# Kernel optimization log

Hardware: AMD Instinct MI355X
Metric: run time of the kernel (lower is better)

## Reference

```python
import jax, jax.numpy as jnp
import numpy as np

ALPHA = 0.2  # leaky relu slope
NEG_BIG = -9e15


def setup_inputs() -> dict:
    key = jax.random.key(0)
    k1, k2, k3, k4 = jax.random.split(key, 4)
    B, N, Fin, Fout = 8, 2048, 128, 128
    h = jax.random.normal(k1, (B, N, Fin), dtype=jnp.float32)
    adj = jax.random.randint(k2, (N, N), 0, 2, dtype=jnp.int32)
    # xavier_uniform with gain=1.414
    limW = 1.414 * np.sqrt(6.0 / (Fin + Fout))
    W = jax.random.uniform(k3, (Fin, Fout), minval=-limW, maxval=limW, dtype=jnp.float32)
    lima = 1.414 * np.sqrt(6.0 / (2 * Fout + 1))
    a = jax.random.uniform(k4, (2 * Fout, 1), minval=-lima, maxval=lima, dtype=jnp.float32)
    return {"h": h, "adj": adj, "W": W, "a": a}


def reference(h, adj, W, a):
    # Wh: [B, N, F]
    Wh = jnp.einsum("bnf,fo->bno", h, W)
    Fout = W.shape[1]
    a1, a2 = a[:Fout, 0], a[Fout:, 0]  # [F], [F]
    # Additive score decomposition (same math as concat trick):
    # e[b,i,j] = leakyrelu(Wh_i . a1 + Wh_j . a2)
    s1 = Wh @ a1  # [B, N] (source/query part)
    s2 = Wh @ a2  # [B, N] (target part)
    e = s1[:, :, None] + s2[:, None, :]  # [B, N, N]
    e = jnp.where(e > 0, e, ALPHA * e)   # leaky relu
    e = jnp.where(adj[None, :, :] > 0, e, NEG_BIG)
    attention = jax.nn.softmax(e, axis=2)  # [B, N, N]
    # dropout is identity in eval mode
    h_prime = jnp.einsum("bij,bjf->bif", attention, Wh)
    return h_prime
```

## Files before the change

### kernel.cpp

```cpp
#include <hip/hip_runtime.h>
#include <hip/hip_bf16.h>
#include <stdint.h>

#define ALPHA 0.2f

typedef __attribute__((ext_vector_type(8))) short bf16x8;
typedef __attribute__((ext_vector_type(4))) float f32x4;

__device__ __forceinline__ short f2bf(float f) {
    union { float f; uint32_t u; } c; c.f = f;
    uint32_t u = c.u + 0x7FFF + ((c.u >> 16) & 1);
    return (short)(u >> 16);
}

__device__ __forceinline__ uint32_t pk_bf16(float lo, float hi) {
    union { float f; uint32_t u; } a, b;
    a.f = lo; b.f = hi;
    return __builtin_amdgcn_perm(b.u + 0x8000u, a.u + 0x8000u, 0x07060302u);
}

__device__ __forceinline__ void gload_lds16(const void* g, void* l) {
    __builtin_amdgcn_global_load_lds(
        (const __attribute__((address_space(1))) void*)g,
        (__attribute__((address_space(3))) void*)l, 16, 0, 0);
}

__global__ __launch_bounds__(256) void pack_adj_kernel(
        const int* __restrict__ adj, uint8_t* __restrict__ bytes,
        const float* __restrict__ W, short* __restrict__ WTg) {
    int t = blockIdx.x * 256 + threadIdx.x;
    const int4* a4 = reinterpret_cast<const int4*>(adj) + (size_t)t * 2;
    int4 x0 = a4[0], x1 = a4[1];
    uint32_t m = 0;
    m |= (x0.x > 0) ? 1u   : 0u;  m |= (x0.y > 0) ? 2u   : 0u;
    m |= (x0.z > 0) ? 4u   : 0u;  m |= (x0.w > 0) ? 8u   : 0u;
    m |= (x1.x > 0) ? 16u  : 0u;  m |= (x1.y > 0) ? 32u  : 0u;
    m |= (x1.z > 0) ? 64u  : 0u;  m |= (x1.w > 0) ? 128u : 0u;
    bytes[t] = (uint8_t)m;

    if (blockIdx.x < 64) {
        int idx = blockIdx.x * 256 + threadIdx.x;
        int k = idx >> 7, f = idx & 127;
        WTg[f * 128 + k] = f2bf(W[k * 128 + f]);
    }
}

__global__ __launch_bounds__(256) void wh_kernel(
        const float* __restrict__ h, const short* __restrict__ WTg,
        const float* __restrict__ a, short* __restrict__ whT,
        float* __restrict__ s1g, float* __restrict__ s2g) {
    __shared__ float sred[4][2][16];
    __shared__ short tr[4][32][24];

    int tid = threadIdx.x, wid = tid >> 6, lane = tid & 63;
    int q = lane >> 4, n = lane & 15;
    int bb = blockIdx.x & 7;
    int tile = blockIdx.x >> 3;
    int rb = bb * 2048 + tile * 16;
    int row = rb + n;

    f32x4 acc[2] = {};
    #pragma unroll
    for (int kc = 0; kc < 4; ++kc) {
        const float* hp = h + (size_t)row * 128 + kc * 32 + q * 8;
        float4 h0 = reinterpret_cast<const float4*>(hp)[0];
        float4 h1 = reinterpret_cast<const float4*>(hp)[1];
        bf16x8 afrag;
        afrag[0] = f2bf(h0.x); afrag[1] = f2bf(h0.y);
        afrag[2] = f2bf(h0.z); afrag[3] = f2bf(h0.w);
        afrag[4] = f2bf(h1.x); afrag[5] = f2bf(h1.y);
        afrag[6] = f2bf(h1.z); afrag[7] = f2bf(h1.w);
        #pragma unroll
        for (int u = 0; u < 2; ++u) {
            int t = wid * 2 + u;
            bf16x8 bfrag = *reinterpret_cast<const bf16x8*>(
                WTg + (t * 16 + n) * 128 + kc * 32 + q * 8);
            acc[u] = __builtin_amdgcn_mfma_f32_16x16x32_bf16(afrag, bfrag, acc[u], 0, 0, 0);
        }
    }

    float p1[4] = {0.f, 0.f, 0.f, 0.f}, p2[4] = {0.f, 0.f, 0.f, 0.f};
    #pragma unroll
    for (int u = 0; u < 2; ++u) {
        int c = (wid * 2 + u) * 16 + n;
        float a1c = a[c], a2c = a[128 + c];
        #pragma unroll
        for (int r = 0; r < 4; ++r) {
            p1[r] += acc[u][r] * a1c;
            p2[r] += acc[u][r] * a2c;
        }
    }
    #pragma unroll
    for (int d = 1; d < 16; d <<= 1) {
        #pragma unroll
        for (int r = 0; r < 4; ++r) {
            p1[r] += __shfl_xor(p1[r], d);
            p2[r] += __shfl_xor(p2[r], d);
        }
    }
    if (n == 0) {
        #pragma unroll
        for (int r = 0; r < 4; ++r) {
            sred[wid][0][q * 4 + r] = p1[r];
            sred[wid][1][q * 4 + r] = p2[r];
        }
    }

    #pragma unroll
    for (int u = 0; u < 2; ++u)
        #pragma unroll
        for (int r = 0; r < 4; ++r)
            tr[wid][u * 16 + n][q * 4 + r] = f2bf(acc[u][r]);
    __syncthreads();

    if (wid == 0 && lane < 16) {
        float v1 = 0.f, v2 = 0.f;
        #pragma unroll
        for (int v = 0; v < 4; ++v) { v1 += sred[v][0][lane]; v2 += sred[v][1][lane]; }
        s1g[rb + lane] = v1;
        s2g[rb + lane] = v2;
    }

    int jr = rb & 2047;
    int fl = lane & 31, jh = lane >> 5;
    bf16x8 v = *reinterpret_cast<const bf16x8*>(&tr[wid][fl][jh * 8]);
    int f = wid * 32 + fl;
    int t = f >> 4, nn = f & 15;
    int jc = jr >> 5;
    int qg = ((jr & 31) >> 3) + jh;
    *reinterpret_cast<bf16x8*>(
        whT + (size_t)(bb * 64 + jc) * 4096 + t * 512 + qg * 128 + nn * 8) = v;
}

__global__ __launch_bounds__(256) void attn_kernel(
        const short* __restrict__ whT, const float* __restrict__ s1g,
        const float* __restrict__ s2g, const uint8_t* __restrict__ adjb,
        float* __restrict__ out) {
    __shared__ char sbuf[2][32768];

    int wid = threadIdx.x >> 6, lane = threadIdx.x & 63;
    int q = lane >> 4, n = lane & 15;
    int b  = blockIdx.x & 7;
    int ib = (blockIdx.x >> 3) * 64;
    int rowA = ib + wid * 16 + n;

    float s1A = s1g[b * 2048 + rowA];
    const float* s2b = s2g + b * 2048;
    const uint32_t* admA = reinterpret_cast<const uint32_t*>(
        adjb + (size_t)rowA * 256);
    const char* gbase = reinterpret_cast<const char*>(whT) + (size_t)b * 524288;

    f32x4 acc[8] = {};
    float ds = 0.f;

    uint32_t mw[4];
    float4 s2l[4], s2h[4];
    #pragma unroll
    for (int u = 0; u < 4; ++u) {
        mw[u] = admA[u];
        s2l[u] = *reinterpret_cast<const float4*>(s2b + u * 32 + q * 8);
        s2h[u] = *reinterpret_cast<const float4*>(s2b + u * 32 + q * 8 + 4);
    }

    {
        const char* g = gbase + wid * 8192 + lane * 16;
        char* l = &sbuf[0][wid * 8192];
        #pragma unroll
        for (int i = 0; i < 8; ++i)
            gload_lds16(g + i * 1024, l + i * 1024);
    }
    __syncthreads();

    for (int s = 0; s < 16; ++s) {
        int cur = s & 1;
        if (s < 15) {
            const char* g = gbase + (size_t)(s + 1) * 32768 + wid * 8192 + lane * 16;
            char* l = &sbuf[cur ^ 1][wid * 8192];
            #pragma unroll
            for (int i = 0; i < 8; ++i)
                gload_lds16(g + i * 1024, l + i * 1024);
        }
        const char* lb = sbuf[cur];
        #pragma unroll
        for (int u = 0; u < 4; ++u) {
            int c = s * 4 + u;
            bf16x8 nb[8];
            const char* cb = lb + u * 8192 + lane * 16;
            #pragma unroll
            for (int t = 0; t < 8; ++t)
                nb[t] = *reinterpret_cast<const bf16x8*>(cb + t * 1024);

            uint32_t mA = mw[u] >> (q * 8);
            float s2arr[8] = {s2l[u].x, s2l[u].y, s2l[u].z, s2l[u].w,
                              s2h[u].x, s2h[u].y, s2h[u].z, s2h[u].w};

            int cn = c + 4; if (cn > 63) cn = 63;
            mw[u] = admA[cn];
            s2l[u] = *reinterpret_cast<const float4*>(s2b + cn * 32 + q * 8);
            s2h[u] = *reinterpret_cast<const float4*>(s2b + cn * 32 + q * 8 + 4);

            float p[8];
            #pragma unroll
            for (int j = 0; j < 8; ++j) {
                float e = s1A + s2arr[j];
                e = fmaxf(e, ALPHA * e);
                float v = ((mA >> j) & 1) ? __expf(e) : 0.0f;
                ds += v; p[j] = v;
            }
            union { uint32_t u32[4]; bf16x8 v; } cv;
            #pragma unroll
            for (int pp = 0; pp < 4; ++pp)
                cv.u32[pp] = pk_bf16(p[2 * pp], p[2 * pp + 1]);

            #pragma unroll
            for (int t = 0; t < 8; ++t)
                acc[t] = __builtin_amdgcn_mfma_f32_16x16x32_bf16(cv.v, nb[t], acc[t], 0, 0, 0);
        }
        __syncthreads();
    }

    ds += __shfl_xor(ds, 16); ds += __shfl_xor(ds, 32);
    float rd[4];
    #pragma unroll
    for (int r = 0; r < 4; ++r) rd[r] = 1.0f / __shfl(ds, q * 4 + r);

    size_t ob = ((size_t)b * 2048 + ib + wid * 16) * 128;
    #pragma unroll
    for (int t = 0; t < 8; ++t)
        #pragma unroll
        for (int r = 0; r < 4; ++r)
            out[ob + (size_t)(q * 4 + r) * 128 + t * 16 + n] = acc[t][r] * rd[r];
}

extern "C" void kernel_launch(void* const* d_in, const int* in_sizes, int n_in,
                              void* d_out, int out_size, void* d_ws, size_t ws_size,
                              hipStream_t stream) {
    const float* h   = (const float*)d_in[0];
    const int*   adj = (const int*)d_in[1];
    const float* W   = (const float*)d_in[2];
    const float* a   = (const float*)d_in[3];
    float* out = (float*)d_out;

    char* ws = (char*)d_ws;
    short* whT = (short*)ws;
    float* s1  = (float*)(ws + 4194304);
    float* s2  = (float*)(ws + 4259840);
    uint8_t* bytes = (uint8_t*)(ws + 4325376);

    short* WTg = (short*)d_out + (4194304 - 16384);

    pack_adj_kernel<<<2048, 256, 0, stream>>>(adj, bytes, W, WTg);
    wh_kernel<<<1024, 256, 0, stream>>>(h, WTg, a, whT, s1, s2);
    attn_kernel<<<256, 256, 0, stream>>>(whT, s1, s2, bytes, out);
}
```

Measured before the change: 114.6 us.

## Stage adjacency mask and s2 in LDS and deepen whT pipeline to four stages

The attention kernel now preloads the block's 64 rows of packed adjacency bits and the full s2 vector into shared memory once, instead of issuing per-iteration global loads for them. The whT streaming changes from a double buffer of 32KB chunks to a 4-deep ring of 8KB chunks, with one chunk processed per iteration and manual vmcnt waits plus raw s_barrier in place of __syncthreads. The intent is to hide global-memory latency with finer-grained prefetch and fewer scalar/vector global loads in the inner loop. In exchange there are four times as many barriers, and correctness depends on the hand-written waitcnt counts, for example at the clamped tail where the last chunk is reloaded.

```diff
diff --git a/kernel.cpp b/kernel.cpp
--- a/kernel.cpp
+++ b/kernel.cpp
@@ -136,9 +136,11 @@
         const short* __restrict__ whT, const float* __restrict__ s1g,
         const float* __restrict__ s2g, const uint8_t* __restrict__ adjb,
         float* __restrict__ out) {
-    __shared__ char sbuf[2][32768];
-
-    int wid = threadIdx.x >> 6, lane = threadIdx.x & 63;
+    __shared__ char sbuf[4][8192];
+    __shared__ uint32_t mlds[64 * 65];
+    __shared__ float s2lds[2048];
+
+    int tid = threadIdx.x, wid = tid >> 6, lane = tid & 63;
     int q = lane >> 4, n = lane & 15;
     int b  = blockIdx.x & 7;
     int ib = (blockIdx.x >> 3) * 64;
@@ -146,77 +148,81 @@
 
     float s1A = s1g[b * 2048 + rowA];
     const float* s2b = s2g + b * 2048;
-    const uint32_t* admA = reinterpret_cast<const uint32_t*>(
-        adjb + (size_t)rowA * 256);
     const char* gbase = reinterpret_cast<const char*>(whT) + (size_t)b * 524288;
+
+    {
+        int rt = tid >> 2, seg = tid & 3;
+        const uint4* src = reinterpret_cast<const uint4*>(
+            adjb + (size_t)(ib + rt) * 256 + seg * 64);
+        uint32_t* dst = &mlds[rt * 65 + seg * 16];
+        #pragma unroll
+        for (int i = 0; i < 4; ++i) {
+            uint4 v = src[i];
+            dst[i * 4 + 0] = v.x; dst[i * 4 + 1] = v.y;
+            dst[i * 4 + 2] = v.z; dst[i * 4 + 3] = v.w;
+        }
+    }
+    {
+        float4 v0 = *reinterpret_cast<const float4*>(s2b + tid * 8);
+        float4 v1 = *reinterpret_cast<const float4*>(s2b + tid * 8 + 4);
+        *reinterpret_cast<float4*>(&s2lds[tid * 8])     = v0;
+        *reinterpret_cast<float4*>(&s2lds[tid * 8 + 4]) = v1;
+    }
+
+    #pragma unroll
+    for (int s0 = 0; s0 < 3; ++s0) {
+        const char* g = gbase + s0 * 8192 + wid * 2048 + lane * 16;
+        char* l = &sbuf[s0][wid * 2048];
+        gload_lds16(g, l);
+        gload_lds16(g + 1024, l + 1024);
+    }
+    asm volatile("s_waitcnt vmcnt(4) lgkmcnt(0)" ::: "memory");
+    asm volatile("s_barrier" ::: "memory");
 
     f32x4 acc[8] = {};
     float ds = 0.f;
-
-    uint32_t mw[4];
-    float4 s2l[4], s2h[4];
-    #pragma unroll
-    for (int u = 0; u < 4; ++u) {
-        mw[u] = admA[u];
-        s2l[u] = *reinterpret_cast<const float4*>(s2b + u * 32 + q * 8);
-        s2h[u] = *reinterpret_cast<const float4*>(s2b + u * 32 + q * 8 + 4);
-    }
-
-    {
-        const char* g = gbase + wid * 8192 + lane * 16;
-        char* l = &sbuf[0][wid * 8192];
-        #pragma unroll
-        for (int i = 0; i < 8; ++i)
-            gload_lds16(g + i * 1024, l + i * 1024);
-    }
-    __syncthreads();
-
-    for (int s = 0; s < 16; ++s) {
-        int cur = s & 1;
-        if (s < 15) {
-            const char* g = gbase + (size_t)(s + 1) * 32768 + wid * 8192 + lane * 16;
-            char* l = &sbuf[cur ^ 1][wid * 8192];
-            #pragma unroll
-            for (int i = 0; i < 8; ++i)
-                gload_lds16(g + i * 1024, l + i * 1024);
-        }
-        const char* lb = sbuf[cur];
-        #pragma unroll
-        for (int u = 0; u < 4; ++u) {
-            int c = s * 4 + u;
-            bf16x8 nb[8];
-            const char* cb = lb + u * 8192 + lane * 16;
-            #pragma unroll
-            for (int t = 0; t < 8; ++t)
-                nb[t] = *reinterpret_cast<const bf16x8*>(cb + t * 1024);
-
-            uint32_t mA = mw[u] >> (q * 8);
-            float s2arr[8] = {s2l[u].x, s2l[u].y, s2l[u].z, s2l[u].w,
-                              s2h[u].x, s2h[u].y, s2h[u].z, s2h[u].w};
-
-            int cn = c + 4; if (cn > 63) cn = 63;
-            mw[u] = admA[cn];
-            s2l[u] = *reinterpret_cast<const float4*>(s2b + cn * 32 + q * 8);
-            s2h[u] = *reinterpret_cast<const float4*>(s2b + cn * 32 + q * 8 + 4);
-
-            float p[8];
-            #pragma unroll
-            for (int j = 0; j < 8; ++j) {
-                float e = s1A + s2arr[j];
-                e = fmaxf(e, ALPHA * e);
-                float v = ((mA >> j) & 1) ? __expf(e) : 0.0f;
-                ds += v; p[j] = v;
-            }
-            union { uint32_t u32[4]; bf16x8 v; } cv;
-            #pragma unroll
-            for (int pp = 0; pp < 4; ++pp)
-                cv.u32[pp] = pk_bf16(p[2 * pp], p[2 * pp + 1]);
-
-            #pragma unroll
-            for (int t = 0; t < 8; ++t)
-                acc[t] = __builtin_amdgcn_mfma_f32_16x16x32_bf16(cv.v, nb[t], acc[t], 0, 0, 0);
-        }
-        __syncthreads();
+    int mbase = (wid * 16 + n) * 65;
+
+    for (int s = 0; s < 64; ++s) {
+        int sn = (s + 3 <= 63) ? s + 3 : 63;
+        {
+            const char* g = gbase + (size_t)sn * 8192 + wid * 2048 + lane * 16;
+            char* l = &sbuf[(s + 3) & 3][wid * 2048];
+            gload_lds16(g, l);
+            gload_lds16(g + 1024, l + 1024);
+        }
+
+        const char* cb = &sbuf[s & 3][0] + lane * 16;
+        bf16x8 nb[8];
+        #pragma unroll
+        for (int t = 0; t < 8; ++t)
+            nb[t] = *reinterpret_cast<const bf16x8*>(cb + t * 1024);
+
+        uint32_t mA = mlds[mbase + s] >> (q * 8);
+        float4 s2a = *reinterpret_cast<const float4*>(&s2lds[s * 32 + q * 8]);
+        float4 s2c = *reinterpret_cast<const float4*>(&s2lds[s * 32 + q * 8 + 4]);
+        float s2arr[8] = {s2a.x, s2a.y, s2a.z, s2a.w,
+                          s2c.x, s2c.y, s2c.z, s2c.w};
+
+        float p[8];
+        #pragma unroll
+        for (int j = 0; j < 8; ++j) {
+            float e = s1A + s2arr[j];
+            e = fmaxf(e, ALPHA * e);
+            float v = ((mA >> j) & 1) ? __expf(e) : 0.0f;
+            ds += v; p[j] = v;
+        }
+        union { uint32_t u32[4]; bf16x8 v; } cv;
+        #pragma unroll
+        for (int pp = 0; pp < 4; ++pp)
+            cv.u32[pp] = pk_bf16(p[2 * pp], p[2 * pp + 1]);
+
+        #pragma unroll
+        for (int t = 0; t < 8; ++t)
+            acc[t] = __builtin_amdgcn_mfma_f32_16x16x32_bf16(cv.v, nb[t], acc[t], 0, 0, 0);
+
+        asm volatile("s_waitcnt vmcnt(4)" ::: "memory");
+        asm volatile("s_barrier" ::: "memory");
     }
 
     ds += __shfl_xor(ds, 16); ds += __shfl_xor(ds, 32);
```

Measured after the change: 120.2 us. +4.9%, slower.
